# Kernel tuning notes

Hardware: AMD Instinct MI355X
Metric: run time of the kernel (lower is better)

The kernel has to match this reference:

```python
import jax, jax.numpy as jnp
import numpy as np

B, S, D = 4096, 200, 64
NUM_USERS = 100000
NUM_ITEMS = 100000


def setup_inputs() -> dict:
    key = jax.random.key(0)
    ks = jax.random.split(key, 16)
    inp = {
        "user_ids": jax.random.randint(ks[0], (B,), 0, NUM_USERS),
        "item_ids": jax.random.randint(ks[1], (B,), 0, NUM_ITEMS),
        "behavior_sequences": jax.random.randint(ks[2], (B, S), 0, NUM_ITEMS),
        # embedding tables
        "user_table": jax.random.normal(ks[3], (NUM_USERS, D), jnp.float32) * 0.02,
        "item_table": jax.random.normal(ks[4], (NUM_ITEMS, D), jnp.float32) * 0.02,
        # attention MLP: Linear(4D, 80) -> ReLU -> Linear(80, 1)
        "att_w1": jax.random.normal(ks[5], (4 * D, 80), jnp.float32) * 0.05,
        "att_b1": jnp.zeros((80,), jnp.float32),
        "att_w2": jax.random.normal(ks[6], (80, 1), jnp.float32) * 0.1,
        "att_b2": jnp.zeros((1,), jnp.float32),
        # predictor MLP: Linear(2D,64)->ReLU->Linear(64,32)->ReLU->Linear(32,1)->Sigmoid
        "pred_w1": jax.random.normal(ks[7], (2 * D, 64), jnp.float32) * 0.08,
        "pred_b1": jnp.zeros((64,), jnp.float32),
        "pred_w2": jax.random.normal(ks[8], (64, 32), jnp.float32) * 0.12,
        "pred_b2": jnp.zeros((32,), jnp.float32),
        "pred_w3": jax.random.normal(ks[9], (32, 1), jnp.float32) * 0.17,
        "pred_b3": jnp.zeros((1,), jnp.float32),
    }
    return inp


def reference(user_ids, item_ids, behavior_sequences,
              user_table, item_table,
              att_w1, att_b1, att_w2, att_b2,
              pred_w1, pred_b1, pred_w2, pred_b2, pred_w3, pred_b3):
    user_emb = user_table[user_ids]                 # (B, D)
    item_emb = item_table[item_ids]                 # (B, D)
    behavior_emb = item_table[behavior_sequences]   # (B, S, D)

    target = item_emb[:, None, :]                   # (B, 1, D) broadcast over S
    product = behavior_emb * target
    subtract = behavior_emb - target
    target_exp = jnp.broadcast_to(target, behavior_emb.shape)
    feats = jnp.concatenate([behavior_emb, target_exp, product, subtract], axis=-1)  # (B, S, 4D)

    h = jax.nn.relu(feats @ att_w1 + att_b1)        # (B, S, 80)
    scores = (h @ att_w2 + att_b2)[..., 0]          # (B, S)
    attn = jax.nn.softmax(scores, axis=1)           # (B, S)

    pooled = jnp.einsum("bsd,bs->bd", behavior_emb, attn)  # (B, D)

    x = jnp.concatenate([user_emb, pooled], axis=-1)        # (B, 2D)
    x = jax.nn.relu(x @ pred_w1 + pred_b1)
    x = jax.nn.relu(x @ pred_w2 + pred_b2)
    out = jax.nn.sigmoid(x @ pred_w3 + pred_b3)             # (B, 1)
    return out
```

## Files before the change

kernel.cpp:

```cpp
#include <hip/hip_runtime.h>
#include <hip/hip_bf16.h>


typedef __attribute__((ext_vector_type(8))) short          bf16x8;
typedef __attribute__((ext_vector_type(8))) unsigned short u16x8;
typedef __attribute__((ext_vector_type(4))) float          f32x4;

__device__ __forceinline__ int swz_gran(int row, int g) {
    return row * 64 + ((g ^ (row & 7)) << 3);
}
__device__ __forceinline__ int swz_elem(int row, int col) {
    return row * 64 + (((col >> 3) ^ (row & 7)) << 3) + (col & 7);
}

extern "C" __global__ __launch_bounds__(256)
void din_prep(const int* __restrict__ item_ids,
              const float* __restrict__ item_table,
              const float* __restrict__ att_w1,
              const float* __restrict__ att_b1,
              __hip_bfloat16* __restrict__ gcb,
              float* __restrict__ bias_out)
{
    const int t   = threadIdx.x;
    const int blk = blockIdx.x;
    if (blk >= 2048) {
        const int i = (blk - 2048) * 256 + t;
        if (i < 64 * 80) {
            const int d = i / 80;
            const int j = i - d * 80;
            const float g = att_w1[d * 80 + j] + att_w1[(192 + d) * 80 + j];
            const float c = att_w1[(128 + d) * 80 + j];
            gcb[swz_elem(j, d)]        = __float2bfloat16(g);
            gcb[5120 + swz_elem(j, d)] = __float2bfloat16(c);
        }
        return;
    }
    if (t < 160) {
        const int bl = t / 80;
        const int jj = t - bl * 80;
        const int b  = blk * 2 + bl;
        const int iid = item_ids[b];
        const float* tgt = item_table + (size_t)iid * 64;
        float acc = att_b1[jj];
        #pragma unroll 4
        for (int d = 0; d < 64; ++d)
            acc = fmaf(tgt[d],
                       att_w1[(64 + d) * 80 + jj] - att_w1[(192 + d) * 80 + jj],
                       acc);
        bias_out[(size_t)b * 80 + jj] = acc;
    }
}

struct __align__(16) LdsW {
    unsigned short gcb[10240];
    float w2[80];
    float biasw[4][80];
    float wsc[4][208];
    float aux[4][128];
    float h1s[4][64];
};

extern "C" __global__ __launch_bounds__(256, 4)
void din_main(const int* __restrict__ user_ids,
              const int* __restrict__ item_ids,
              const int* __restrict__ seq,
              const float* __restrict__ user_table,
              const float* __restrict__ item_table,
              const float* __restrict__ att_w2,
              const float* __restrict__ pred_w1,
              const float* __restrict__ pred_b1,
              const float* __restrict__ pred_w2,
              const float* __restrict__ pred_b2,
              const float* __restrict__ pred_w3,
              const float* __restrict__ pred_b3,
              const unsigned short* __restrict__ gcb_g,
              const float* __restrict__ bias_g,
              float* __restrict__ out)
{
    __shared__ LdsW L;
    const int t  = threadIdx.x;
    const int wv = t >> 6;
    const int l  = t & 63;
    const int lr = l & 15;
    const int ks = l >> 4;
    const int b  = blockIdx.x * 4 + wv;

    {
        const u16x8* src = reinterpret_cast<const u16x8*>(gcb_g);
        u16x8* dst = reinterpret_cast<u16x8*>(L.gcb);
        #pragma unroll
        for (int i = 0; i < 5; ++i) dst[t + i * 256] = src[t + i * 256];
    }
    if (t < 80) L.w2[t] = att_w2[t];
    L.biasw[wv][l] = bias_g[(size_t)b * 80 + l];
    if (l < 16) L.biasw[wv][64 + l] = bias_g[(size_t)b * 80 + 64 + l];

    const int iid = item_ids[b];
    const float4* tp = reinterpret_cast<const float4*>(
        item_table + (size_t)iid * 64);
    const float4 tg0 = tp[2 * ks], tg1 = tp[2 * ks + 1];
    const float4 tg2 = tp[8 + 2 * ks], tg3 = tp[8 + 2 * ks + 1];
    const int uid = user_ids[b];
    const float uem = user_table[(size_t)uid * 64 + l];
    const int* seqb = seq + b * 200;

    __syncthreads();

    float bias_r[5], w2_r[5];
    #pragma unroll
    for (int nt = 0; nt < 5; ++nt) {
        bias_r[nt] = L.biasw[wv][nt * 16 + lr];
        w2_r[nt]   = L.w2[nt * 16 + lr];
    }

    float pl[8], ph[8];
    #pragma unroll
    for (int e = 0; e < 8; ++e) { pl[e] = 0.f; ph[e] = 0.f; }
    float mrun = -1e30f, ssum = 0.f;

    for (int mt = 0; mt < 13; ++mt) {
        const int srow = mt * 16 + lr;
        const bool val = srow < 200;
        const int row = val ? seqb[srow] : 0;
        const float4* rp = reinterpret_cast<const float4*>(
            item_table + (size_t)row * 64);
        float4 q0 = rp[2 * ks], q1 = rp[2 * ks + 1];
        float4 q2 = rp[8 + 2 * ks], q3 = rp[8 + 2 * ks + 1];
        if (!val) {
            q0 = make_float4(0.f, 0.f, 0.f, 0.f);
            q1 = make_float4(0.f, 0.f, 0.f, 0.f);
            q2 = make_float4(0.f, 0.f, 0.f, 0.f);
            q3 = make_float4(0.f, 0.f, 0.f, 0.f);
        }
        union { u16x8 u; bf16x8 bf; __hip_bfloat162 h2[4]; } A0, A1, A2, A3;
        A0.h2[0] = __float22bfloat162_rn(float2{q0.x, q0.y});
        A0.h2[1] = __float22bfloat162_rn(float2{q0.z, q0.w});
        A0.h2[2] = __float22bfloat162_rn(float2{q1.x, q1.y});
        A0.h2[3] = __float22bfloat162_rn(float2{q1.z, q1.w});
        A1.h2[0] = __float22bfloat162_rn(float2{q2.x, q2.y});
        A1.h2[1] = __float22bfloat162_rn(float2{q2.z, q2.w});
        A1.h2[2] = __float22bfloat162_rn(float2{q3.x, q3.y});
        A1.h2[3] = __float22bfloat162_rn(float2{q3.z, q3.w});
        A2.h2[0] = __float22bfloat162_rn(float2{q0.x * tg0.x, q0.y * tg0.y});
        A2.h2[1] = __float22bfloat162_rn(float2{q0.z * tg0.z, q0.w * tg0.w});
        A2.h2[2] = __float22bfloat162_rn(float2{q1.x * tg1.x, q1.y * tg1.y});
        A2.h2[3] = __float22bfloat162_rn(float2{q1.z * tg1.z, q1.w * tg1.w});
        A3.h2[0] = __float22bfloat162_rn(float2{q2.x * tg2.x, q2.y * tg2.y});
        A3.h2[1] = __float22bfloat162_rn(float2{q2.z * tg2.z, q2.w * tg2.w});
        A3.h2[2] = __float22bfloat162_rn(float2{q3.x * tg3.x, q3.y * tg3.y});
        A3.h2[3] = __float22bfloat162_rn(float2{q3.z * tg3.z, q3.w * tg3.w});

        f32x4 acc[5];
        #pragma unroll
        for (int nt = 0; nt < 5; ++nt)
            acc[nt] = (f32x4){0.f, 0.f, 0.f, 0.f};
        #pragma unroll
        for (int nt = 0; nt < 5; ++nt) {
            const int j = nt * 16 + lr;
            const bf16x8 g0 = *reinterpret_cast<const bf16x8*>(
                &L.gcb[swz_gran(j, ks)]);
            const bf16x8 g1 = *reinterpret_cast<const bf16x8*>(
                &L.gcb[swz_gran(j, 4 + ks)]);
            const bf16x8 c0 = *reinterpret_cast<const bf16x8*>(
                &L.gcb[5120 + swz_gran(j, ks)]);
            const bf16x8 c1 = *reinterpret_cast<const bf16x8*>(
                &L.gcb[5120 + swz_gran(j, 4 + ks)]);
            acc[nt] = __builtin_amdgcn_mfma_f32_16x16x32_bf16(A0.bf, g0, acc[nt], 0, 0, 0);
            acc[nt] = __builtin_amdgcn_mfma_f32_16x16x32_bf16(A1.bf, g1, acc[nt], 0, 0, 0);
            acc[nt] = __builtin_amdgcn_mfma_f32_16x16x32_bf16(A2.bf, c0, acc[nt], 0, 0, 0);
            acc[nt] = __builtin_amdgcn_mfma_f32_16x16x32_bf16(A3.bf, c1, acc[nt], 0, 0, 0);
        }

        float pv[4];
        #pragma unroll
        for (int r = 0; r < 4; ++r) {
            const int s = mt * 16 + ks * 4 + r;
            float p = 0.f;
            #pragma unroll
            for (int nt = 0; nt < 5; ++nt)
                p += fmaxf(acc[nt][r] + bias_r[nt], 0.f) * w2_r[nt];
            p += __shfl_xor(p, 1);
            p += __shfl_xor(p, 2);
            p += __shfl_xor(p, 4);
            p += __shfl_xor(p, 8);
            if (s >= 200) p = -1e30f;
            pv[r] = p;
            if (lr == 0 && s < 200) L.wsc[wv][s] = p;
        }
        float tmax = fmaxf(fmaxf(pv[0], pv[1]), fmaxf(pv[2], pv[3]));
        tmax = fmaxf(tmax, __shfl_xor(tmax, 16));
        tmax = fmaxf(tmax, __shfl_xor(tmax, 32));
        if (tmax > mrun) {
            const float sc = __expf(mrun - tmax);
            #pragma unroll
            for (int e = 0; e < 8; ++e) { pl[e] *= sc; ph[e] *= sc; }
            ssum *= sc;
            mrun = tmax;
        }
        float w = 0.f;
        if (val) w = __expf(L.wsc[wv][srow] - mrun);
        ssum += w;
        pl[0] = fmaf(w, q0.x, pl[0]); pl[1] = fmaf(w, q0.y, pl[1]);
        pl[2] = fmaf(w, q0.z, pl[2]); pl[3] = fmaf(w, q0.w, pl[3]);
        pl[4] = fmaf(w, q1.x, pl[4]); pl[5] = fmaf(w, q1.y, pl[5]);
        pl[6] = fmaf(w, q1.z, pl[6]); pl[7] = fmaf(w, q1.w, pl[7]);
        ph[0] = fmaf(w, q2.x, ph[0]); ph[1] = fmaf(w, q2.y, ph[1]);
        ph[2] = fmaf(w, q2.z, ph[2]); ph[3] = fmaf(w, q2.w, ph[3]);
        ph[4] = fmaf(w, q3.x, ph[4]); ph[5] = fmaf(w, q3.y, ph[5]);
        ph[6] = fmaf(w, q3.z, ph[6]); ph[7] = fmaf(w, q3.w, ph[7]);
    }

    #pragma unroll
    for (int msk = 1; msk < 16; msk <<= 1) {
        #pragma unroll
        for (int e = 0; e < 8; ++e) {
            pl[e] += __shfl_xor(pl[e], msk);
            ph[e] += __shfl_xor(ph[e], msk);
        }
        ssum += __shfl_xor(ssum, msk);
    }
    const float inv = 1.f / ssum;
    if (lr == 0) {
        #pragma unroll
        for (int e = 0; e < 8; ++e) {
            L.aux[wv][64 + 8 * ks + e]      = pl[e] * inv;
            L.aux[wv][64 + 32 + 8 * ks + e] = ph[e] * inv;
        }
    }
    L.aux[wv][l] = uem;

    float a0 = pred_b1[l], a1 = 0.f, a2 = 0.f, a3 = 0.f;
    #pragma unroll 4
    for (int k = 0; k < 128; k += 4) {
        a0 = fmaf(L.aux[wv][k],     pred_w1[k * 64 + l],       a0);
        a1 = fmaf(L.aux[wv][k + 1], pred_w1[(k + 1) * 64 + l], a1);
        a2 = fmaf(L.aux[wv][k + 2], pred_w1[(k + 2) * 64 + l], a2);
        a3 = fmaf(L.aux[wv][k + 3], pred_w1[(k + 3) * 64 + l], a3);
    }
    L.h1s[wv][l] = fmaxf((a0 + a1) + (a2 + a3), 0.f);
    const int j2 = l & 31;
    float c0 = pred_b2[j2], c1 = 0.f;
    #pragma unroll 4
    for (int k = 0; k < 64; k += 2) {
        c0 = fmaf(L.h1s[wv][k],     pred_w2[k * 32 + j2],       c0);
        c1 = fmaf(L.h1s[wv][k + 1], pred_w2[(k + 1) * 32 + j2], c1);
    }
    float p = fmaxf(c0 + c1, 0.f) * pred_w3[j2];
    p += __shfl_xor(p, 1);
    p += __shfl_xor(p, 2);
    p += __shfl_xor(p, 4);
    p += __shfl_xor(p, 8);
    p += __shfl_xor(p, 16);
    if (l == 0) {
        const float z = p + pred_b3[0];
        out[b] = 1.f / (1.f + __expf(-z));
    }
}

extern "C" void kernel_launch(void* const* d_in, const int* in_sizes, int n_in,
                              void* d_out, int out_size, void* d_ws, size_t ws_size,
                              hipStream_t stream)
{
    const int*   user_ids   = (const int*)  d_in[0];
    const int*   item_ids   = (const int*)  d_in[1];
    const int*   seq        = (const int*)  d_in[2];
    const float* user_table = (const float*)d_in[3];
    const float* item_table = (const float*)d_in[4];
    const float* att_w1     = (const float*)d_in[5];
    const float* att_b1     = (const float*)d_in[6];
    const float* att_w2     = (const float*)d_in[7];
    const float* pred_w1    = (const float*)d_in[9];
    const float* pred_b1    = (const float*)d_in[10];
    const float* pred_w2    = (const float*)d_in[11];
    const float* pred_b2    = (const float*)d_in[12];
    const float* pred_w3    = (const float*)d_in[13];
    const float* pred_b3    = (const float*)d_in[14];
    float* out = (float*)d_out;

    __hip_bfloat16* gcb = (__hip_bfloat16*)d_ws;
    float* bias_ws = (float*)((char*)d_ws + 20480);

    din_prep<<<2068, 256, 0, stream>>>(item_ids, item_table, att_w1, att_b1,
                                       gcb, bias_ws);
    din_main<<<1024, 256, 0, stream>>>(user_ids, item_ids, seq,
                                       user_table, item_table, att_w2,
                                       pred_w1, pred_b1, pred_w2, pred_b2,
                                       pred_w3, pred_b3,
                                       (const unsigned short*)gcb, bias_ws,
                                       out);
}
```

Baseline: 69.77 us.

## Split each batch row's sequence across two waves with online-softmax merge

Each batch row is now processed by two wavefronts that handle alternating 16-row tiles of the behavior sequence, so each block covers 2 rows instead of 4 and the grid grows to 2048 blocks. The two partial softmax states (running max, sum and weighted pooled vectors) go to LDS and are merged after a barrier, then one wave runs the predictor MLP. Occupancy is raised to 6 blocks per SM. The aim is more parallelism and shorter per-wave serial loops, at the cost of loading the gcb weights into LDS twice as often, one extra block barrier, and half the waves sitting idle during the MLP tail.

```diff
diff --git a/kernel.cpp b/kernel.cpp
--- a/kernel.cpp
+++ b/kernel.cpp
@@ -54,13 +54,15 @@
 struct __align__(16) LdsW {
     unsigned short gcb[10240];
     float w2[80];
-    float biasw[4][80];
-    float wsc[4][208];
-    float aux[4][128];
-    float h1s[4][64];
+    float biasw[2][80];
+    float wsc[2][208];
+    float mpool[2][2][4][16];
+    float mms[2][2][2];
+    float aux[2][128];
+    float h1s[2][64];
 };
 
-extern "C" __global__ __launch_bounds__(256, 4)
+extern "C" __global__ __launch_bounds__(256, 6)
 void din_main(const int* __restrict__ user_ids,
               const int* __restrict__ item_ids,
               const int* __restrict__ seq,
@@ -78,12 +80,14 @@
               float* __restrict__ out)
 {
     __shared__ LdsW L;
-    const int t  = threadIdx.x;
-    const int wv = t >> 6;
-    const int l  = t & 63;
-    const int lr = l & 15;
-    const int ks = l >> 4;
-    const int b  = blockIdx.x * 4 + wv;
+    const int t    = threadIdx.x;
+    const int wv   = t >> 6;
+    const int bb   = wv >> 1;
+    const int half = wv & 1;
+    const int l    = t & 63;
+    const int lr   = l & 15;
+    const int ks   = l >> 4;
+    const int b    = blockIdx.x * 2 + bb;
 
     {
         const u16x8* src = reinterpret_cast<const u16x8*>(gcb_g);
@@ -92,8 +96,10 @@
         for (int i = 0; i < 5; ++i) dst[t + i * 256] = src[t + i * 256];
     }
     if (t < 80) L.w2[t] = att_w2[t];
-    L.biasw[wv][l] = bias_g[(size_t)b * 80 + l];
-    if (l < 16) L.biasw[wv][64 + l] = bias_g[(size_t)b * 80 + 64 + l];
+    if (half == 0) {
+        L.biasw[bb][l] = bias_g[(size_t)b * 80 + l];
+        if (l < 16) L.biasw[bb][64 + l] = bias_g[(size_t)b * 80 + 64 + l];
+    }
 
     const int iid = item_ids[b];
     const float4* tp = reinterpret_cast<const float4*>(
@@ -109,7 +115,7 @@
     float bias_r[5], w2_r[5];
     #pragma unroll
     for (int nt = 0; nt < 5; ++nt) {
-        bias_r[nt] = L.biasw[wv][nt * 16 + lr];
+        bias_r[nt] = L.biasw[bb][nt * 16 + lr];
         w2_r[nt]   = L.w2[nt * 16 + lr];
     }
 
@@ -118,7 +124,7 @@
     for (int e = 0; e < 8; ++e) { pl[e] = 0.f; ph[e] = 0.f; }
     float mrun = -1e30f, ssum = 0.f;
 
-    for (int mt = 0; mt < 13; ++mt) {
+    for (int mt = half; mt < 13; mt += 2) {
         const int srow = mt * 16 + lr;
         const bool val = srow < 200;
         const int row = val ? seqb[srow] : 0;
@@ -185,7 +191,7 @@
             p += __shfl_xor(p, 8);
             if (s >= 200) p = -1e30f;
             pv[r] = p;
-            if (lr == 0 && s < 200) L.wsc[wv][s] = p;
+            if (lr == 0 && s < 200) L.wsc[bb][s] = p;
         }
         float tmax = fmaxf(fmaxf(pv[0], pv[1]), fmaxf(pv[2], pv[3]));
         tmax = fmaxf(tmax, __shfl_xor(tmax, 16));
@@ -198,7 +204,7 @@
             mrun = tmax;
         }
         float w = 0.f;
-        if (val) w = __expf(L.wsc[wv][srow] - mrun);
+        if (val) w = __expf(L.wsc[bb][srow] - mrun);
         ssum += w;
         pl[0] = fmaf(w, q0.x, pl[0]); pl[1] = fmaf(w, q0.y, pl[1]);
         pl[2] = fmaf(w, q0.z, pl[2]); pl[3] = fmaf(w, q0.w, pl[3]);
@@ -219,41 +225,65 @@
         }
         ssum += __shfl_xor(ssum, msk);
     }
-    const float inv = 1.f / ssum;
+
     if (lr == 0) {
         #pragma unroll
         for (int e = 0; e < 8; ++e) {
-            L.aux[wv][64 + 8 * ks + e]      = pl[e] * inv;
-            L.aux[wv][64 + 32 + 8 * ks + e] = ph[e] * inv;
-        }
-    }
-    L.aux[wv][l] = uem;
-
-    float a0 = pred_b1[l], a1 = 0.f, a2 = 0.f, a3 = 0.f;
-    #pragma unroll 4
-    for (int k = 0; k < 128; k += 4) {
-        a0 = fmaf(L.aux[wv][k],     pred_w1[k * 64 + l],       a0);
-        a1 = fmaf(L.aux[wv][k + 1], pred_w1[(k + 1) * 64 + l], a1);
-        a2 = fmaf(L.aux[wv][k + 2], pred_w1[(k + 2) * 64 + l], a2);
-        a3 = fmaf(L.aux[wv][k + 3], pred_w1[(k + 3) * 64 + l], a3);
-    }
-    L.h1s[wv][l] = fmaxf((a0 + a1) + (a2 + a3), 0.f);
-    const int j2 = l & 31;
-    float c0 = pred_b2[j2], c1 = 0.f;
-    #pragma unroll 4
-    for (int k = 0; k < 64; k += 2) {
-        c0 = fmaf(L.h1s[wv][k],     pred_w2[k * 32 + j2],       c0);
-        c1 = fmaf(L.h1s[wv][k + 1], pred_w2[(k + 1) * 32 + j2], c1);
-    }
-    float p = fmaxf(c0 + c1, 0.f) * pred_w3[j2];
-    p += __shfl_xor(p, 1);
-    p += __shfl_xor(p, 2);
-    p += __shfl_xor(p, 4);
-    p += __shfl_xor(p, 8);
-    p += __shfl_xor(p, 16);
+            L.mpool[bb][half][ks][e]     = pl[e];
+            L.mpool[bb][half][ks][8 + e] = ph[e];
+        }
+    }
     if (l == 0) {
-        const float z = p + pred_b3[0];
-        out[b] = 1.f / (1.f + __expf(-z));
+        L.mms[bb][half][0] = mrun;
+        L.mms[bb][half][1] = ssum;
+    }
+    __syncthreads();
+
+    if (half == 0) {
+        const float m0 = L.mms[bb][0][0], s0 = L.mms[bb][0][1];
+        const float m1 = L.mms[bb][1][0], s1 = L.mms[bb][1][1];
+        const float ms = fmaxf(m0, m1);
+        const float e0 = __expf(m0 - ms), e1 = __expf(m1 - ms);
+        const float inv = 1.f / (s0 * e0 + s1 * e1);
+        if (lr == 0) {
+            #pragma unroll
+            for (int e = 0; e < 8; ++e) {
+                L.aux[bb][64 + 8 * ks + e] =
+                    (L.mpool[bb][0][ks][e] * e0 +
+                     L.mpool[bb][1][ks][e] * e1) * inv;
+                L.aux[bb][64 + 32 + 8 * ks + e] =
+                    (L.mpool[bb][0][ks][8 + e] * e0 +
+                     L.mpool[bb][1][ks][8 + e] * e1) * inv;
+            }
+        }
+        L.aux[bb][l] = uem;
+
+        float a0 = pred_b1[l], a1 = 0.f, a2 = 0.f, a3 = 0.f;
+        #pragma unroll 4
+        for (int k = 0; k < 128; k += 4) {
+            a0 = fmaf(L.aux[bb][k],     pred_w1[k * 64 + l],       a0);
+            a1 = fmaf(L.aux[bb][k + 1], pred_w1[(k + 1) * 64 + l], a1);
+            a2 = fmaf(L.aux[bb][k + 2], pred_w1[(k + 2) * 64 + l], a2);
+            a3 = fmaf(L.aux[bb][k + 3], pred_w1[(k + 3) * 64 + l], a3);
+        }
+        L.h1s[bb][l] = fmaxf((a0 + a1) + (a2 + a3), 0.f);
+        const int j2 = l & 31;
+        float c0 = pred_b2[j2], c1 = 0.f;
+        #pragma unroll 4
+        for (int k = 0; k < 64; k += 2) {
+            c0 = fmaf(L.h1s[bb][k],     pred_w2[k * 32 + j2],       c0);
+            c1 = fmaf(L.h1s[bb][k + 1], pred_w2[(k + 1) * 32 + j2], c1);
+        }
+        float p = fmaxf(c0 + c1, 0.f) * pred_w3[j2];
+        p += __shfl_xor(p, 1);
+        p += __shfl_xor(p, 2);
+        p += __shfl_xor(p, 4);
+        p += __shfl_xor(p, 8);
+        p += __shfl_xor(p, 16);
+        if (l == 0) {
+            const float z = p + pred_b3[0];
+            out[b] = 1.f / (1.f + __expf(-z));
+        }
     }
 }
 
@@ -282,7 +312,7 @@
 
     din_prep<<<2068, 256, 0, stream>>>(item_ids, item_table, att_w1, att_b1,
                                        gcb, bias_ws);
-    din_main<<<1024, 256, 0, stream>>>(user_ids, item_ids, seq,
+    din_main<<<2048, 256, 0, stream>>>(user_ids, item_ids, seq,
                                        user_table, item_table, att_w2,
                                        pred_w1, pred_b1, pred_w2, pred_b2,
                                        pred_w3, pred_b3,
```

Result: slower. 158.8 us (+127.6%).

## Convert item table to bf16 in prep and gather bf16 rows in main kernel

Applied to the files above, without the earlier changes.

The prep kernel gains extra blocks that convert the whole 100k x 64 fp32 item table to bf16 in workspace. A new main kernel gathers behavior and target rows from that bf16 copy, halving the bytes per random gather, and feeds them straight to the MFMA operands. Converting the full table every call costs about 25.6 MB of read and 12.8 MB of write, which may exceed the savings on roughly 820k gathered rows. It also lowers the precision of the pooled embeddings, and the old fp32 path is kept as a fallback when workspace is too small.

```diff
diff --git a/kernel.cpp b/kernel.cpp
--- a/kernel.cpp
+++ b/kernel.cpp
@@ -6,11 +6,16 @@
 typedef __attribute__((ext_vector_type(8))) unsigned short u16x8;
 typedef __attribute__((ext_vector_type(4))) float          f32x4;
 
+#define NITEMS 100000
+
 __device__ __forceinline__ int swz_gran(int row, int g) {
     return row * 64 + ((g ^ (row & 7)) << 3);
 }
 __device__ __forceinline__ int swz_elem(int row, int col) {
     return row * 64 + (((col >> 3) ^ (row & 7)) << 3) + (col & 7);
+}
+__device__ __forceinline__ float bits2f(unsigned int u) {
+    union { unsigned int u; float f; } v; v.u = u; return v.f;
 }
 
 extern "C" __global__ __launch_bounds__(256)
@@ -19,10 +24,26 @@
               const float* __restrict__ att_w1,
               const float* __restrict__ att_b1,
               __hip_bfloat16* __restrict__ gcb,
-              float* __restrict__ bias_out)
+              float* __restrict__ bias_out,
+              unsigned short* __restrict__ tbl16)
 {
     const int t   = threadIdx.x;
     const int blk = blockIdx.x;
+    if (blk >= 2068) {
+        const int i = (blk - 2068) * 256 + t;
+        if (i < NITEMS * 8) {
+            const float4* s = reinterpret_cast<const float4*>(item_table) + i * 2;
+            const float4 p0 = s[0];
+            const float4 p1 = s[1];
+            union { u16x8 v; __hip_bfloat162 h2[4]; } cv;
+            cv.h2[0] = __float22bfloat162_rn(float2{p0.x, p0.y});
+            cv.h2[1] = __float22bfloat162_rn(float2{p0.z, p0.w});
+            cv.h2[2] = __float22bfloat162_rn(float2{p1.x, p1.y});
+            cv.h2[3] = __float22bfloat162_rn(float2{p1.z, p1.w});
+            *reinterpret_cast<u16x8*>(tbl16 + (size_t)i * 8) = cv.v;
+        }
+        return;
+    }
     if (blk >= 2048) {
         const int i = (blk - 2048) * 256 + t;
         if (i < 64 * 80) {
@@ -61,21 +82,215 @@
 };
 
 extern "C" __global__ __launch_bounds__(256, 4)
-void din_main(const int* __restrict__ user_ids,
-              const int* __restrict__ item_ids,
-              const int* __restrict__ seq,
-              const float* __restrict__ user_table,
-              const float* __restrict__ item_table,
-              const float* __restrict__ att_w2,
-              const float* __restrict__ pred_w1,
-              const float* __restrict__ pred_b1,
-              const float* __restrict__ pred_w2,
-              const float* __restrict__ pred_b2,
-              const float* __restrict__ pred_w3,
-              const float* __restrict__ pred_b3,
-              const unsigned short* __restrict__ gcb_g,
-              const float* __restrict__ bias_g,
-              float* __restrict__ out)
+void din_main_bt(const int* __restrict__ user_ids,
+                 const int* __restrict__ item_ids,
+                 const int* __restrict__ seq,
+                 const float* __restrict__ user_table,
+                 const float* __restrict__ att_w2,
+                 const float* __restrict__ pred_w1,
+                 const float* __restrict__ pred_b1,
+                 const float* __restrict__ pred_w2,
+                 const float* __restrict__ pred_b2,
+                 const float* __restrict__ pred_w3,
+                 const float* __restrict__ pred_b3,
+                 const unsigned short* __restrict__ gcb_g,
+                 const float* __restrict__ bias_g,
+                 const unsigned short* __restrict__ tbl,
+                 float* __restrict__ out)
+{
+    __shared__ LdsW L;
+    const int t  = threadIdx.x;
+    const int wv = t >> 6;
+    const int l  = t & 63;
+    const int lr = l & 15;
+    const int ks = l >> 4;
+    const int b  = blockIdx.x * 4 + wv;
+
+    {
+        const u16x8* src = reinterpret_cast<const u16x8*>(gcb_g);
+        u16x8* dst = reinterpret_cast<u16x8*>(L.gcb);
+        #pragma unroll
+        for (int i = 0; i < 5; ++i) dst[t + i * 256] = src[t + i * 256];
+    }
+    if (t < 80) L.w2[t] = att_w2[t];
+    L.biasw[wv][l] = bias_g[(size_t)b * 80 + l];
+    if (l < 16) L.biasw[wv][64 + l] = bias_g[(size_t)b * 80 + 64 + l];
+
+    const int iid = item_ids[b];
+    const unsigned short* tbt = tbl + (size_t)iid * 64;
+    const u16x8 tA = *reinterpret_cast<const u16x8*>(tbt + 8 * ks);
+    const u16x8 tB = *reinterpret_cast<const u16x8*>(tbt + 32 + 8 * ks);
+    float tgl[8], tgh[8];
+    #pragma unroll
+    for (int e = 0; e < 8; ++e) {
+        tgl[e] = bits2f((unsigned int)tA[e] << 16);
+        tgh[e] = bits2f((unsigned int)tB[e] << 16);
+    }
+    const int uid = user_ids[b];
+    const float uem = user_table[(size_t)uid * 64 + l];
+    const int* seqb = seq + b * 200;
+
+    __syncthreads();
+
+    float bias_r[5], w2_r[5];
+    #pragma unroll
+    for (int nt = 0; nt < 5; ++nt) {
+        bias_r[nt] = L.biasw[wv][nt * 16 + lr];
+        w2_r[nt]   = L.w2[nt * 16 + lr];
+    }
+
+    float pl[8], ph[8];
+    #pragma unroll
+    for (int e = 0; e < 8; ++e) { pl[e] = 0.f; ph[e] = 0.f; }
+    float mrun = -1e30f, ssum = 0.f;
+
+    for (int mt = 0; mt < 13; ++mt) {
+        const int srow = mt * 16 + lr;
+        const bool val = srow < 200;
+        const int row = val ? seqb[srow] : 0;
+        const unsigned short* rp = tbl + (size_t)row * 64;
+        u16x8 a0 = *reinterpret_cast<const u16x8*>(rp + 8 * ks);
+        u16x8 a1 = *reinterpret_cast<const u16x8*>(rp + 32 + 8 * ks);
+        if (!val) { a0 = (u16x8)0; a1 = (u16x8)0; }
+
+        float b0f[8], b1f[8];
+        #pragma unroll
+        for (int e = 0; e < 8; ++e) {
+            b0f[e] = bits2f((unsigned int)a0[e] << 16);
+            b1f[e] = bits2f((unsigned int)a1[e] << 16);
+        }
+        union { u16x8 u; bf16x8 bf; __hip_bfloat162 h2[4]; } A2, A3;
+        A2.h2[0] = __float22bfloat162_rn(float2{b0f[0] * tgl[0], b0f[1] * tgl[1]});
+        A2.h2[1] = __float22bfloat162_rn(float2{b0f[2] * tgl[2], b0f[3] * tgl[3]});
+        A2.h2[2] = __float22bfloat162_rn(float2{b0f[4] * tgl[4], b0f[5] * tgl[5]});
+        A2.h2[3] = __float22bfloat162_rn(float2{b0f[6] * tgl[6], b0f[7] * tgl[7]});
+        A3.h2[0] = __float22bfloat162_rn(float2{b1f[0] * tgh[0], b1f[1] * tgh[1]});
+        A3.h2[1] = __float22bfloat162_rn(float2{b1f[2] * tgh[2], b1f[3] * tgh[3]});
+        A3.h2[2] = __float22bfloat162_rn(float2{b1f[4] * tgh[4], b1f[5] * tgh[5]});
+        A3.h2[3] = __float22bfloat162_rn(float2{b1f[6] * tgh[6], b1f[7] * tgh[7]});
+        const bf16x8 A0 = *reinterpret_cast<const bf16x8*>(&a0);
+        const bf16x8 A1 = *reinterpret_cast<const bf16x8*>(&a1);
+
+        f32x4 acc[5];
+        #pragma unroll
+        for (int nt = 0; nt < 5; ++nt)
+            acc[nt] = (f32x4){0.f, 0.f, 0.f, 0.f};
+        #pragma unroll
+        for (int nt = 0; nt < 5; ++nt) {
+            const int j = nt * 16 + lr;
+            const bf16x8 g0 = *reinterpret_cast<const bf16x8*>(
+                &L.gcb[swz_gran(j, ks)]);
+            const bf16x8 g1 = *reinterpret_cast<const bf16x8*>(
+                &L.gcb[swz_gran(j, 4 + ks)]);
+            const bf16x8 c0 = *reinterpret_cast<const bf16x8*>(
+                &L.gcb[5120 + swz_gran(j, ks)]);
+            const bf16x8 c1 = *reinterpret_cast<const bf16x8*>(
+                &L.gcb[5120 + swz_gran(j, 4 + ks)]);
+            acc[nt] = __builtin_amdgcn_mfma_f32_16x16x32_bf16(A0,    g0, acc[nt], 0, 0, 0);
+            acc[nt] = __builtin_amdgcn_mfma_f32_16x16x32_bf16(A1,    g1, acc[nt], 0, 0, 0);
+            acc[nt] = __builtin_amdgcn_mfma_f32_16x16x32_bf16(A2.bf, c0, acc[nt], 0, 0, 0);
+            acc[nt] = __builtin_amdgcn_mfma_f32_16x16x32_bf16(A3.bf, c1, acc[nt], 0, 0, 0);
+        }
+
+        float pv[4];
+        #pragma unroll
+        for (int r = 0; r < 4; ++r) {
+            const int s = mt * 16 + ks * 4 + r;
+            float p = 0.f;
+            #pragma unroll
+            for (int nt = 0; nt < 5; ++nt)
+                p += fmaxf(acc[nt][r] + bias_r[nt], 0.f) * w2_r[nt];
+            p += __shfl_xor(p, 1);
+            p += __shfl_xor(p, 2);
+            p += __shfl_xor(p, 4);
+            p += __shfl_xor(p, 8);
+            if (s >= 200) p = -1e30f;
+            pv[r] = p;
+            if (lr == 0 && s < 200) L.wsc[wv][s] = p;
+        }
+        float tmax = fmaxf(fmaxf(pv[0], pv[1]), fmaxf(pv[2], pv[3]));
+        tmax = fmaxf(tmax, __shfl_xor(tmax, 16));
+        tmax = fmaxf(tmax, __shfl_xor(tmax, 32));
+        if (tmax > mrun) {
+            const float sc = __expf(mrun - tmax);
+            #pragma unroll
+            for (int e = 0; e < 8; ++e) { pl[e] *= sc; ph[e] *= sc; }
+            ssum *= sc;
+            mrun = tmax;
+        }
+        float w = 0.f;
+        if (val) w = __expf(L.wsc[wv][srow] - mrun);
+        ssum += w;
+        #pragma unroll
+        for (int e = 0; e < 8; ++e) {
+            pl[e] = fmaf(w, b0f[e], pl[e]);
+            ph[e] = fmaf(w, b1f[e], ph[e]);
+        }
+    }
+
+    #pragma unroll
+    for (int msk = 1; msk < 16; msk <<= 1) {
+        #pragma unroll
+        for (int e = 0; e < 8; ++e) {
+            pl[e] += __shfl_xor(pl[e], msk);
+            ph[e] += __shfl_xor(ph[e], msk);
+        }
+        ssum += __shfl_xor(ssum, msk);
+    }
+    const float inv = 1.f / ssum;
+    if (lr == 0) {
+        #pragma unroll
+        for (int e = 0; e < 8; ++e) {
+            L.aux[wv][64 + 8 * ks + e]      = pl[e] * inv;
+            L.aux[wv][64 + 32 + 8 * ks + e] = ph[e] * inv;
+        }
+    }
+    L.aux[wv][l] = uem;
+
+    float a0r = pred_b1[l], a1r = 0.f, a2r = 0.f, a3r = 0.f;
+    #pragma unroll 4
+    for (int k = 0; k < 128; k += 4) {
+        a0r = fmaf(L.aux[wv][k],     pred_w1[k * 64 + l],       a0r);
+        a1r = fmaf(L.aux[wv][k + 1], pred_w1[(k + 1) * 64 + l], a1r);
+        a2r = fmaf(L.aux[wv][k + 2], pred_w1[(k + 2) * 64 + l], a2r);
+        a3r = fmaf(L.aux[wv][k + 3], pred_w1[(k + 3) * 64 + l], a3r);
+    }
+    L.h1s[wv][l] = fmaxf((a0r + a1r) + (a2r + a3r), 0.f);
+    const int j2 = l & 31;
+    float c0r = pred_b2[j2], c1r = 0.f;
+    #pragma unroll 4
+    for (int k = 0; k < 64; k += 2) {
+        c0r = fmaf(L.h1s[wv][k],     pred_w2[k * 32 + j2],       c0r);
+        c1r = fmaf(L.h1s[wv][k + 1], pred_w2[(k + 1) * 32 + j2], c1r);
+    }
+    float p = fmaxf(c0r + c1r, 0.f) * pred_w3[j2];
+    p += __shfl_xor(p, 1);
+    p += __shfl_xor(p, 2);
+    p += __shfl_xor(p, 4);
+    p += __shfl_xor(p, 8);
+    p += __shfl_xor(p, 16);
+    if (l == 0) {
+        const float z = p + pred_b3[0];
+        out[b] = 1.f / (1.f + __expf(-z));
+    }
+}
+
+extern "C" __global__ __launch_bounds__(256, 4)
+void din_main_f32(const int* __restrict__ user_ids,
+                  const int* __restrict__ item_ids,
+                  const int* __restrict__ seq,
+                  const float* __restrict__ user_table,
+                  const float* __restrict__ item_table,
+                  const float* __restrict__ att_w2,
+                  const float* __restrict__ pred_w1,
+                  const float* __restrict__ pred_b1,
+                  const float* __restrict__ pred_w2,
+                  const float* __restrict__ pred_b2,
+                  const float* __restrict__ pred_w3,
+                  const float* __restrict__ pred_b3,
+                  const unsigned short* __restrict__ gcb_g,
+                  const float* __restrict__ bias_g,
+                  float* __restrict__ out)
 {
     __shared__ LdsW L;
     const int t  = threadIdx.x;
@@ -277,15 +492,29 @@
     const float* pred_b3    = (const float*)d_in[14];
     float* out = (float*)d_out;
 
-    __hip_bfloat16* gcb = (__hip_bfloat16*)d_ws;
-    float* bias_ws = (float*)((char*)d_ws + 20480);
-
-    din_prep<<<2068, 256, 0, stream>>>(item_ids, item_table, att_w1, att_b1,
-                                       gcb, bias_ws);
-    din_main<<<1024, 256, 0, stream>>>(user_ids, item_ids, seq,
-                                       user_table, item_table, att_w2,
-                                       pred_w1, pred_b1, pred_w2, pred_b2,
-                                       pred_w3, pred_b3,
-                                       (const unsigned short*)gcb, bias_ws,
-                                       out);
-}
+    char* ws = (char*)d_ws;
+    __hip_bfloat16* gcb      = (__hip_bfloat16*)ws;
+    float*          bias_ws  = (float*)(ws + 20480);
+    unsigned short* tbl16    = (unsigned short*)(ws + 20480 + 1310720);
+    const size_t NEED = 20480 + 1310720 + (size_t)NITEMS * 64 * 2;
+
+    if (ws_size >= NEED) {
+        din_prep<<<5193, 256, 0, stream>>>(item_ids, item_table, att_w1,
+                                           att_b1, gcb, bias_ws, tbl16);
+        din_main_bt<<<1024, 256, 0, stream>>>(user_ids, item_ids, seq,
+                                              user_table, att_w2,
+                                              pred_w1, pred_b1, pred_w2,
+                                              pred_b2, pred_w3, pred_b3,
+                                              (const unsigned short*)gcb,
+                                              bias_ws, tbl16, out);
+    } else {
+        din_prep<<<2068, 256, 0, stream>>>(item_ids, item_table, att_w1,
+                                           att_b1, gcb, bias_ws, tbl16);
+        din_main_f32<<<1024, 256, 0, stream>>>(user_ids, item_ids, seq,
+                                               user_table, item_table, att_w2,
+                                               pred_w1, pred_b1, pred_w2,
+                                               pred_b2, pred_w3, pred_b3,
+                                               (const unsigned short*)gcb,
+                                               bias_ws, out);
+    }
+}
```

Result: faster. 62.02 us, median of 2 (-11.1%).
